# Optimization experiments

Hardware: AMD Instinct MI355X
Metric: run time of the kernel (lower is better)

The kernel has to match this reference:

```python
import jax, jax.numpy as jnp
import numpy as np

B, N, D = 4, 2048, 512      # batch, seq, dim_in
DK = DV = 512               # dim_k == dim_v (required by fc input width)
NH = 8
HK = DK // NH               # per-head dk == dv == 64
SCALE = 1.0 / np.sqrt(HK)
LN_EPS = 1e-5


def setup_inputs() -> dict:
    key = jax.random.key(0)
    ks = jax.random.split(key, 8)
    s = 0.02
    return {
        "x": jax.random.normal(ks[0], (B, N, D), dtype=jnp.float32),
        "Wq": jax.random.normal(ks[1], (D, DK), dtype=jnp.float32) * s,
        "Wk": jax.random.normal(ks[2], (D, DK), dtype=jnp.float32) * s,
        "Wv": jax.random.normal(ks[3], (D, DV), dtype=jnp.float32) * s,
        "Wf": jax.random.normal(ks[4], (2 * DK, D), dtype=jnp.float32) * s,
        "bf": jnp.zeros((D,), dtype=jnp.float32),
        "gamma": jnp.ones((D,), dtype=jnp.float32),
        "beta": jnp.zeros((D,), dtype=jnp.float32),
    }


def reference(x, Wq, Wk, Wv, Wf, bf, gamma, beta):
    b, n, _ = x.shape
    # projections -> [b, nh, n, hk]; q_c/q_f etc. are identical in the source,
    # so compute once.
    def proj(W):
        return jnp.einsum('bnd,dk->bnk', x, W).reshape(b, n, NH, -1).transpose(0, 2, 1, 3)
    q, k, v = proj(Wq), proj(Wk), proj(Wv)

    # conventional branch: softmax over n x n scores
    dist_c = jax.nn.softmax(jnp.einsum('bhqd,bhkd->bhqk', q, k) * SCALE, axis=-1)
    att_c = jnp.einsum('bhqk,bhkd->bhqd', dist_c, v)          # [b,nh,n,hk]
    att_c = att_c.transpose(0, 2, 1, 3).reshape(b, n, DV)

    # feature branch: softmax over dk x dk scores (linear-complexity variant)
    dist_f = jax.nn.softmax(jnp.einsum('bhnk,bhnq->bhkq', k, q) * SCALE, axis=-1)
    att_f = jnp.einsum('bhnd,bhdq->bhnq', v, dist_f)           # [b,nh,n,hk]
    att_f = att_f.transpose(0, 2, 1, 3).reshape(b, n, DV)

    att = jnp.concatenate([att_c, att_f], axis=2)              # [b,n,2*dk]
    out = jax.nn.relu(att @ Wf + bf)                           # dropout=eval (identity)
    out = out + x
    mu = jnp.mean(out, axis=-1, keepdims=True)
    var = jnp.var(out, axis=-1, keepdims=True)
    out = (out - mu) * jax.lax.rsqrt(var + LN_EPS) * gamma + beta
    return out
```

## Files before the change

### kernel.cpp

```cpp
#include <hip/hip_runtime.h>
#include <math.h>
#include <stdint.h>

#define B_   4
#define N_   2048
#define D_   512
#define DK_  512
#define NH_  8
#define HK_  64
#define LN_EPS_ 1e-5f
#define QS_  0.18033688011112042f

typedef unsigned short u16;
typedef __attribute__((ext_vector_type(8))) short short8;
typedef __attribute__((ext_vector_type(4))) float f32x4;
typedef __attribute__((ext_vector_type(8))) unsigned short u16x8;

__device__ __forceinline__ u16 f2bf(float x) {
    uint32_t u = __builtin_bit_cast(uint32_t, x);
    return (u16)((u + 0x7fffu + ((u >> 16) & 1u)) >> 16);
}
__device__ __forceinline__ u16 f2bf_fast(float x) {
    return (u16)((__builtin_bit_cast(uint32_t, x) + 0x8000u) >> 16);
}
__device__ __forceinline__ float b2f(u16 v) {
    return __builtin_bit_cast(float, (uint32_t)v << 16);
}
__device__ __forceinline__ uint32_t cvtpk_bf16(float lo, float hi) {
    uint32_t r;
    asm("v_cvt_pk_bf16_f32 %0, %1, %2" : "=v"(r) : "v"(lo), "v"(hi));
    return r;
}
__device__ __forceinline__ float exp2f_fast(float x) {
    return __builtin_amdgcn_exp2f(x);
}

__device__ __forceinline__ void gload16(const void* g, void* l) {
    __builtin_amdgcn_global_load_lds(
        reinterpret_cast<const __attribute__((address_space(1))) void*>(
            reinterpret_cast<uintptr_t>(g)),
        reinterpret_cast<__attribute__((address_space(3))) void*>(
            static_cast<uint32_t>(reinterpret_cast<uintptr_t>(l))),
        16, 0, 0);
}

__global__ __launch_bounds__(256) void prep_kernel(
    const float* __restrict__ x, const float* __restrict__ Wq,
    const float* __restrict__ Wk, const float* __restrict__ Wv,
    const float* __restrict__ Wf, u16* __restrict__ xb,
    u16* __restrict__ wqkvT, u16* __restrict__ wfT)
{
    __shared__ float t[32][33];
    const int bid = blockIdx.x, tid = threadIdx.x;
    if (bid < 2048) {
        const int i = (bid * 256 + tid) * 8;
        const float4 a = *reinterpret_cast<const float4*>(&x[i]);
        const float4 b = *reinterpret_cast<const float4*>(&x[i + 4]);
        u16x8 o;
        o[0] = f2bf(a.x); o[1] = f2bf(a.y); o[2] = f2bf(a.z); o[3] = f2bf(a.w);
        o[4] = f2bf(b.x); o[5] = f2bf(b.y); o[6] = f2bf(b.z); o[7] = f2bf(b.w);
        *reinterpret_cast<u16x8*>(&xb[i]) = o;
        return;
    }
    const float* W;
    u16* dst;
    int K, Nc, nt, kt;
    if (bid < 2816) {
        const int z = (bid - 2048) >> 8, rem = (bid - 2048) & 255;
        W = z == 0 ? Wq : (z == 1 ? Wk : Wv);
        dst = wqkvT + (size_t)z * 512 * 512;
        K = 512; Nc = 512;
        nt = (rem & 15) * 32; kt = (rem >> 4) * 32;
    } else {
        const int rem = bid - 2816;
        W = Wf; dst = wfT; K = 1024; Nc = 512;
        nt = (rem & 15) * 32; kt = (rem >> 4) * 32;
    }
    {
        const int r = tid >> 3, c0 = (tid & 7) * 4;
        const float4 v = *reinterpret_cast<const float4*>(
            &W[(size_t)(kt + r) * Nc + nt + c0]);
        t[r][c0] = v.x; t[r][c0 + 1] = v.y; t[r][c0 + 2] = v.z; t[r][c0 + 3] = v.w;
    }
    __syncthreads();
    {
        const int nidx = tid >> 3, kc = (tid & 7) * 4;
        u16 o[4];
        #pragma unroll
        for (int j = 0; j < 4; ++j) o[j] = f2bf(t[kc + j][nidx]);
        *reinterpret_cast<ushort4*>(&dst[(size_t)(nt + nidx) * K + kt + kc]) =
            make_ushort4(o[0], o[1], o[2], o[3]);
    }
}

template<int BM, int BN, int MODE>
__global__ __launch_bounds__(256) void gemm_bf16(
    const u16* __restrict__ A, const u16* __restrict__ Bt,
    u16* __restrict__ qb, u16* __restrict__ kb,
    u16* __restrict__ vb, u16* __restrict__ vt, int M, int Nc, int K,
    const float* __restrict__ bias, const float* __restrict__ resid)
{
    constexpr int MI = BM / 32, NI = BN / 32;
    constexpr int AL = BM / 32, BL = BN / 32;
    __shared__ u16 As[BM * 64];
    __shared__ u16 Bs[BN * 64];
    const int tid = threadIdx.x;
    const int lane = tid & 63, wave = tid >> 6;
    const int wm = wave >> 1, wn = wave & 1;
    const int l15 = lane & 15, lg = lane >> 4;

    const int nwg = gridDim.x;
    const int bid = ((int)blockIdx.x & 7) * (nwg >> 3) + ((int)blockIdx.x >> 3);
    const int ntiles = Nc / BN;
    const int nt = (bid % ntiles) * BN;
    const int mt = (bid / ntiles) * BM;

    f32x4 acc[MI][NI] = {};

    for (int kt = 0; kt < K; kt += 64) {
        __syncthreads();
        #pragma unroll
        for (int i = 0; i < AL; ++i) {
            const int ob = (wave * AL + i) * 1024;
            const int o = ob + lane * 16;
            const int row = o >> 7;
            const int inner = (o & 127) ^ ((row & 7) << 4);
            gload16((const char*)A + ((size_t)(mt + row) * K + kt) * 2 + inner,
                    (char*)As + ob);
        }
        #pragma unroll
        for (int i = 0; i < BL; ++i) {
            const int ob = (wave * BL + i) * 1024;
            const int o = ob + lane * 16;
            const int row = o >> 7;
            const int inner = (o & 127) ^ ((row & 7) << 4);
            gload16((const char*)Bt + ((size_t)(nt + row) * K + kt) * 2 + inner,
                    (char*)Bs + ob);
        }
        __syncthreads();
        #pragma unroll
        for (int ks = 0; ks < 2; ++ks) {
            const int kb2 = ks * 32 + lg * 8;
            short8 af[MI], bfr[NI];
            #pragma unroll
            for (int mi = 0; mi < MI; ++mi) {
                const int r = wm * (BM / 2) + mi * 16 + l15;
                af[mi] = *reinterpret_cast<const short8*>(
                    &As[r * 64 + (kb2 ^ ((r & 7) << 3))]);
            }
            #pragma unroll
            for (int ni = 0; ni < NI; ++ni) {
                const int r = wn * (BN / 2) + ni * 16 + l15;
                bfr[ni] = *reinterpret_cast<const short8*>(
                    &Bs[r * 64 + (kb2 ^ ((r & 7) << 3))]);
            }
            #pragma unroll
            for (int mi = 0; mi < MI; ++mi)
                #pragma unroll
                for (int ni = 0; ni < NI; ++ni)
                    acc[mi][ni] = __builtin_amdgcn_mfma_f32_16x16x32_bf16(
                        af[mi], bfr[ni], acc[mi][ni], 0, 0, 0);
        }
    }

    #pragma unroll
    for (int mi = 0; mi < MI; ++mi) {
        #pragma unroll
        for (int ni = 0; ni < NI; ++ni) {
            const int col = nt + wn * (BN / 2) + ni * 16 + l15;
            const int row0 = mt + wm * (BM / 2) + mi * 16 + lg * 4;
            if (MODE == 1) {
                if (col < 512) {
                    #pragma unroll
                    for (int jj = 0; jj < 4; ++jj)
                        qb[(size_t)(row0 + jj) * 512 + col] =
                            f2bf(acc[mi][ni][jj] * QS_);
                } else if (col < 1024) {
                    #pragma unroll
                    for (int jj = 0; jj < 4; ++jj)
                        kb[(size_t)(row0 + jj) * 512 + col - 512] =
                            f2bf(acc[mi][ni][jj]);
                } else {
                    const int dfull = col - 1024;
                    const int hh = dfull >> 6, dd = dfull & 63;
                    const int bb = row0 >> 11, nn = row0 & 2047;
                    u16 o4[4];
                    #pragma unroll
                    for (int jj = 0; jj < 4; ++jj) {
                        o4[jj] = f2bf(acc[mi][ni][jj]);
                        vb[(size_t)(row0 + jj) * 512 + dfull] = o4[jj];
                    }
                    *reinterpret_cast<ushort4*>(
                        &vt[(((size_t)(bb * NH_ + hh)) * HK_ + dd) * N_ + nn]) =
                        make_ushort4(o4[0], o4[1], o4[2], o4[3]);
                }
            } else {
                #pragma unroll
                for (int jj = 0; jj < 4; ++jj) {
                    const size_t row = (size_t)(row0 + jj);
                    float v = acc[mi][ni][jj];
                    v += bias[col];
                    v = fmaxf(v, 0.0f);
                    v += resid[row * Nc + col];
                    qb[row * Nc + col] = f2bf(v);
                }
            }
        }
    }
}

__global__ __launch_bounds__(256) void flash_featS_kernel(
    const u16* __restrict__ Qb, const u16* __restrict__ Kb,
    const u16* __restrict__ Vt, u16* __restrict__ att,
    float* __restrict__ partials)
{
    __shared__ u16 sh[24576];
    const int tid = threadIdx.x;
    const int lane = tid & 63, wave = tid >> 6;
    const int l15 = lane & 15, lg = lane >> 4;

    if ((int)blockIdx.x >= 512) {
        u16* KsT = sh;
        u16* QsT = sh + 4096;
        const int fid = (int)blockIdx.x - 512;
        const int ns = fid & 7, h = (fid >> 3) & 7, b = fid >> 6;
        const size_t hbase = (size_t)b * N_ * DK_ + (size_t)h * HK_;

        f32x4 acc[4] = {};
        for (int c = 0; c < 4; ++c) {
            const int n0 = ns * 256 + c * 64;
            __syncthreads();
            #pragma unroll
            for (int it = 0; it < 2; ++it) {
                const int idx = tid + it * 256;
                const int n = idx >> 3, d0 = (idx & 7) * 8;
                const u16x8 kv = *reinterpret_cast<const u16x8*>(
                    &Kb[hbase + (size_t)(n0 + n) * DK_ + d0]);
                const u16x8 qv = *reinterpret_cast<const u16x8*>(
                    &Qb[hbase + (size_t)(n0 + n) * DK_ + d0]);
                #pragma unroll
                for (int j = 0; j < 8; ++j) {
                    const int r = d0 + j;
                    const int cidx = n ^ ((r & 7) << 3);
                    KsT[r * 64 + cidx] = kv[j];
                    QsT[r * 64 + cidx] = qv[j];
                }
            }
            __syncthreads();
            #pragma unroll
            for (int ks = 0; ks < 2; ++ks) {
                const int kb2 = ks * 32 + lg * 8;
                const int ar = wave * 16 + l15;
                const short8 aK = *reinterpret_cast<const short8*>(
                    &KsT[ar * 64 + (kb2 ^ ((ar & 7) << 3))]);
                #pragma unroll
                for (int ni = 0; ni < 4; ++ni) {
                    const int br = ni * 16 + l15;
                    const short8 bQ = *reinterpret_cast<const short8*>(
                        &QsT[br * 64 + (kb2 ^ ((br & 7) << 3))]);
                    acc[ni] = __builtin_amdgcn_mfma_f32_16x16x32_bf16(
                        aK, bQ, acc[ni], 0, 0, 0);
                }
            }
        }
        const int bh = b * NH_ + h;
        #pragma unroll
        for (int ni = 0; ni < 4; ++ni)
            #pragma unroll
            for (int jj = 0; jj < 4; ++jj) {
                const int row = wave * 16 + lg * 4 + jj;
                partials[(((size_t)ns * 32 + bh) * 64 + row) * 64 + ni * 16 + l15] =
                    acc[ni][jj];
            }
        return;
    }

    u16* Ks0 = sh;
    u16* Ks1 = sh + 4096;
    u16* Vs0 = sh + 8192;
    u16* Vs1 = sh + 12288;
    u16* Ps  = sh + 16384;
    const int lbid = (((int)blockIdx.x & 7) << 6) + ((int)blockIdx.x >> 3);
    const int qt = lbid & 15, h = (lbid >> 4) & 7, b = lbid >> 7;

    short8 aq[2][2];
    #pragma unroll
    for (int qs = 0; qs < 2; ++qs) {
        const int qrow = qt * 128 + qs * 64 + wave * 16 + l15;
        const u16* qp = Qb + ((size_t)(b * N_ + qrow)) * DK_ + h * HK_ + lg * 8;
        aq[qs][0] = *reinterpret_cast<const short8*>(qp);
        aq[qs][1] = *reinterpret_cast<const short8*>(qp + 32);
    }
    short8 ones;
    #pragma unroll
    for (int i = 0; i < 8; ++i) ones[i] = (short)0x3F80;

    const u16* Kbase = Kb + (size_t)b * N_ * DK_ + (size_t)h * HK_;
    const u16* Vbase = Vt + ((size_t)(b * NH_ + h)) * HK_ * N_;
    unsigned long long* Ps64 = reinterpret_cast<unsigned long long*>(Ps);

    f32x4 o[2][5] = {};
    float m_[2] = {-1e30f, -1e30f};

#define STAGE(ktile, KBUF, VBUF) do {                                          \
    _Pragma("unroll")                                                          \
    for (int i_ = 0; i_ < 2; ++i_) {                                           \
        const int ob_ = (wave * 2 + i_) * 1024;                                \
        const int oo_ = ob_ + lane * 16;                                       \
        const int row_ = oo_ >> 7;                                             \
        const int inner_ = (oo_ & 127) ^ ((row_ & 7) << 4);                    \
        gload16((const char*)Kbase +                                           \
                    ((size_t)((ktile) * 64 + row_) * DK_) * 2 + inner_,        \
                (char*)(KBUF) + ob_);                                          \
        gload16((const char*)Vbase +                                           \
                    ((size_t)row_ * N_ + (ktile) * 64) * 2 + inner_,           \
                (char*)(VBUF) + ob_);                                          \
    }                                                                          \
} while (0)

#define FLASH_STEP(KBUF, VBUF) do {                                            \
    f32x4 s[2][4] = {};                                                        \
    __builtin_amdgcn_s_setprio(1);                                             \
    _Pragma("unroll")                                                          \
    for (int ks = 0; ks < 2; ++ks) {                                           \
        const int kb2 = ks * 32 + lg * 8;                                      \
        _Pragma("unroll")                                                      \
        for (int t = 0; t < 4; ++t) {                                          \
            const int r = t * 16 + l15;                                        \
            const short8 bk = *reinterpret_cast<const short8*>(                \
                &(KBUF)[r * 64 + (kb2 ^ ((r & 7) << 3))]);                     \
            s[0][t] = __builtin_amdgcn_mfma_f32_16x16x32_bf16(                 \
                bk, aq[0][ks], s[0][t], 0, 0, 0);                              \
            s[1][t] = __builtin_amdgcn_mfma_f32_16x16x32_bf16(                 \
                bk, aq[1][ks], s[1][t], 0, 0, 0);                              \
        }                                                                      \
    }                                                                          \
    __builtin_amdgcn_s_setprio(0);                                             \
    float rmax[2], cm;                                                         \
    _Pragma("unroll")                                                          \
    for (int qs = 0; qs < 2; ++qs) {                                           \
        float a0 = fmaxf(fmaxf(s[qs][0][0], s[qs][0][1]),                      \
                         fmaxf(s[qs][0][2], s[qs][0][3]));                     \
        float a1 = fmaxf(fmaxf(s[qs][1][0], s[qs][1][1]),                      \
                         fmaxf(s[qs][1][2], s[qs][1][3]));                     \
        float a2 = fmaxf(fmaxf(s[qs][2][0], s[qs][2][1]),                      \
                         fmaxf(s[qs][2][2], s[qs][2][3]));                     \
        float a3 = fmaxf(fmaxf(s[qs][3][0], s[qs][3][1]),                      \
                         fmaxf(s[qs][3][2], s[qs][3][3]));                     \
        rmax[qs] = fmaxf(fmaxf(a0, a1), fmaxf(a2, a3));                        \
    }                                                                          \
    cm = fmaxf(rmax[0] - m_[0], rmax[1] - m_[1]);                              \
    if (__any(cm > 8.0f)) {                                                    \
        _Pragma("unroll")                                                      \
        for (int qs = 0; qs < 2; ++qs) {                                       \
            float rm = rmax[qs];                                               \
            rm = fmaxf(rm, __shfl_xor(rm, 16));                                \
            rm = fmaxf(rm, __shfl_xor(rm, 32));                                \
            const float newm = fmaxf(m_[qs], rm);                              \
            const float fac = exp2f_fast(m_[qs] - newm);                       \
            m_[qs] = newm;                                                     \
            float facq[4];                                                     \
            _Pragma("unroll")                                                  \
            for (int jj = 0; jj < 4; ++jj)                                     \
                facq[jj] = __shfl(fac, lg * 4 + jj);                           \
            _Pragma("unroll")                                                  \
            for (int t = 0; t < 5; ++t)                                        \
                _Pragma("unroll")                                              \
                for (int jj = 0; jj < 4; ++jj)                                 \
                    o[qs][t][jj] *= facq[jj];                                  \
        }                                                                      \
    }                                                                          \
    _Pragma("unroll")                                                          \
    for (int qs = 0; qs < 2; ++qs) {                                           \
        const int prow = qs * 64 + wave * 16 + l15;                            \
        const int pb64 = prow * 16;                                            \
        const int sw1 = (prow & 7) << 1;                                       \
        _Pragma("unroll")                                                      \
        for (int t = 0; t < 4; ++t) {                                          \
            const float p0 = exp2f_fast(s[qs][t][0] - m_[qs]);                 \
            const float p1 = exp2f_fast(s[qs][t][1] - m_[qs]);                 \
            const float p2 = exp2f_fast(s[qs][t][2] - m_[qs]);                 \
            const float p3 = exp2f_fast(s[qs][t][3] - m_[qs]);                 \
            const uint32_t lo = cvtpk_bf16(p0, p1);                            \
            const uint32_t hi = cvtpk_bf16(p2, p3);                            \
            Ps64[pb64 + ((t * 4 + lg) ^ sw1)] =                                \
                (unsigned long long)lo | ((unsigned long long)hi << 32);       \
        }                                                                      \
    }                                                                          \
    __builtin_amdgcn_s_setprio(1);                                             \
    _Pragma("unroll")                                                          \
    for (int ks = 0; ks < 2; ++ks) {                                           \
        const int kb2 = ks * 32 + lg * 8;                                      \
        const int pr0 = wave * 16 + l15;                                       \
        const int pr1 = 64 + pr0;                                              \
        const short8 ap0 = *reinterpret_cast<const short8*>(                   \
            &Ps[pr0 * 64 + (kb2 ^ ((pr0 & 7) << 3))]);                         \
        const short8 ap1 = *reinterpret_cast<const short8*>(                   \
            &Ps[pr1 * 64 + (kb2 ^ ((pr1 & 7) << 3))]);                         \
        _Pragma("unroll")                                                      \
        for (int t = 0; t < 4; ++t) {                                          \
            const int dr = t * 16 + l15;                                       \
            const short8 bv = *reinterpret_cast<const short8*>(                \
                &(VBUF)[dr * 64 + (kb2 ^ ((dr & 7) << 3))]);                   \
            o[0][t] = __builtin_amdgcn_mfma_f32_16x16x32_bf16(                 \
                ap0, bv, o[0][t], 0, 0, 0);                                    \
            o[1][t] = __builtin_amdgcn_mfma_f32_16x16x32_bf16(                 \
                ap1, bv, o[1][t], 0, 0, 0);                                    \
        }                                                                      \
        o[0][4] = __builtin_amdgcn_mfma_f32_16x16x32_bf16(                     \
            ap0, ones, o[0][4], 0, 0, 0);                                      \
        o[1][4] = __builtin_amdgcn_mfma_f32_16x16x32_bf16(                     \
            ap1, ones, o[1][4], 0, 0, 0);                                      \
    }                                                                          \
    __builtin_amdgcn_s_setprio(0);                                             \
} while (0)

    STAGE(0, Ks0, Vs0);
    __syncthreads();

    #pragma unroll 1
    for (int kt = 0; kt < N_ / 64; kt += 2) {
        STAGE(kt + 1, Ks1, Vs1);
        FLASH_STEP(Ks0, Vs0);
        __syncthreads();
        if (kt + 2 < N_ / 64) STAGE(kt + 2, Ks0, Vs0);
        FLASH_STEP(Ks1, Vs1);
        __syncthreads();
    }
#undef STAGE
#undef FLASH_STEP

    #pragma unroll
    for (int qs = 0; qs < 2; ++qs)
        #pragma unroll
        for (int jj = 0; jj < 4; ++jj) {
            const float inv = 1.0f / o[qs][4][jj];
            const size_t row = (size_t)b * N_ + qt * 128 + qs * 64 + wave * 16 + lg * 4 + jj;
            #pragma unroll
            for (int t = 0; t < 4; ++t)
                att[row * (2 * DK_) + h * HK_ + t * 16 + l15] =
                    f2bf_fast(o[qs][t][jj] * inv);
        }
}

__global__ __launch_bounds__(256) void featSM_kernel(
    const float* __restrict__ partials, u16* __restrict__ distfT)
{
    const int bh = blockIdx.x, tid = threadIdx.x;
    const int r = tid >> 2, qq = tid & 3;
    float v[16];
    #pragma unroll
    for (int j = 0; j < 16; ++j) v[j] = 0.0f;
    for (int s = 0; s < 8; ++s) {
        const float4* pp = reinterpret_cast<const float4*>(
            &partials[(((size_t)s * 32 + bh) * 64 + r) * 64 + qq * 16]);
        #pragma unroll
        for (int j4 = 0; j4 < 4; ++j4) {
            const float4 a = pp[j4];
            v[j4 * 4 + 0] += a.x; v[j4 * 4 + 1] += a.y;
            v[j4 * 4 + 2] += a.z; v[j4 * 4 + 3] += a.w;
        }
    }
    float m = v[0];
    #pragma unroll
    for (int j = 1; j < 16; ++j) m = fmaxf(m, v[j]);
    m = fmaxf(m, __shfl_xor(m, 1));
    m = fmaxf(m, __shfl_xor(m, 2));
    float sum = 0.0f;
    #pragma unroll
    for (int j = 0; j < 16; ++j) { v[j] = exp2f_fast(v[j] - m); sum += v[j]; }
    sum += __shfl_xor(sum, 1);
    sum += __shfl_xor(sum, 2);
    const float inv = 1.0f / sum;
    #pragma unroll
    for (int j = 0; j < 16; ++j)
        distfT[(size_t)bh * 4096 + (qq * 16 + j) * 64 + r] = f2bf_fast(v[j] * inv);
}

__global__ __launch_bounds__(256) void featAV_mfma(
    const u16* __restrict__ V, const u16* __restrict__ distfT,
    u16* __restrict__ att)
{
    __shared__ u16 Bs[64 * 64];
    __shared__ u16 As[64 * 64];
    const int tid = threadIdx.x;
    const int lane = tid & 63, wave = tid >> 6;
    const int l15 = lane & 15, lg = lane >> 4;
    const int ns = blockIdx.x, h = blockIdx.y, b = blockIdx.z;
    const int bh = b * NH_ + h;

    #pragma unroll
    for (int it = 0; it < 2; ++it) {
        const int idx = tid + it * 256;
        const int r = idx >> 3, c0 = (idx & 7) * 8;
        const u16x8 dv = *reinterpret_cast<const u16x8*>(
            &distfT[(size_t)bh * 4096 + r * 64 + c0]);
        *reinterpret_cast<u16x8*>(&Bs[r * 64 + (c0 ^ ((r & 7) << 3))]) = dv;
    }

    for (int c = 0; c < 4; ++c) {
        const int n0 = ns * 256 + c * 64;
        __syncthreads();
        #pragma unroll
        for (int i = 0; i < 2; ++i) {
            const int ob = (wave * 2 + i) * 1024;
            const int o_ = ob + lane * 16;
            const int row = o_ >> 7;
            const int inner = (o_ & 127) ^ ((row & 7) << 4);
            gload16((const char*)V + ((size_t)(b * N_ + n0 + row) * DK_ + h * HK_) * 2 + inner,
                    (char*)As + ob);
        }
        __syncthreads();
        f32x4 acc[4] = {};
        #pragma unroll
        for (int ks = 0; ks < 2; ++ks) {
            const int kb2 = ks * 32 + lg * 8;
            const int ar = wave * 16 + l15;
            const short8 av = *reinterpret_cast<const short8*>(
                &As[ar * 64 + (kb2 ^ ((ar & 7) << 3))]);
            #pragma unroll
            for (int ni = 0; ni < 4; ++ni) {
                const int br = ni * 16 + l15;
                const short8 bd = *reinterpret_cast<const short8*>(
                    &Bs[br * 64 + (kb2 ^ ((br & 7) << 3))]);
                acc[ni] = __builtin_amdgcn_mfma_f32_16x16x32_bf16(av, bd, acc[ni], 0, 0, 0);
            }
        }
        #pragma unroll
        for (int ni = 0; ni < 4; ++ni)
            #pragma unroll
            for (int jj = 0; jj < 4; ++jj)
                att[((size_t)b * N_ + n0 + wave * 16 + lg * 4 + jj) * (2 * DK_)
                    + 512 + h * HK_ + ni * 16 + l15] = f2bf_fast(acc[ni][jj]);
    }
}

__global__ __launch_bounds__(256) void ln_kernel(
    const u16* __restrict__ fc, const float* __restrict__ gamma,
    const float* __restrict__ beta, float* __restrict__ out)
{
    const int row = blockIdx.x * 4 + (threadIdx.x >> 6);
    const int lane = threadIdx.x & 63;
    const int c = lane * 8;
    const u16x8 v = *reinterpret_cast<const u16x8*>(&fc[(size_t)row * D_ + c]);
    float f[8];
    float s = 0.0f, sq = 0.0f;
    #pragma unroll
    for (int j = 0; j < 8; ++j) {
        f[j] = b2f(v[j]);
        s += f[j];
        sq = fmaf(f[j], f[j], sq);
    }
    #pragma unroll
    for (int off = 32; off >= 1; off >>= 1) {
        s  += __shfl_xor(s, off);
        sq += __shfl_xor(sq, off);
    }
    const float mu = s * (1.0f / D_);
    const float var = sq * (1.0f / D_) - mu * mu;
    const float rstd = rsqrtf(var + LN_EPS_);
    const float4 g0 = *reinterpret_cast<const float4*>(&gamma[c]);
    const float4 g1 = *reinterpret_cast<const float4*>(&gamma[c + 4]);
    const float4 b0 = *reinterpret_cast<const float4*>(&beta[c]);
    const float4 b1 = *reinterpret_cast<const float4*>(&beta[c + 4]);
    const float gg[8] = {g0.x, g0.y, g0.z, g0.w, g1.x, g1.y, g1.z, g1.w};
    const float bb[8] = {b0.x, b0.y, b0.z, b0.w, b1.x, b1.y, b1.z, b1.w};
    float4 o0, o1;
    o0.x = (f[0] - mu) * rstd * gg[0] + bb[0];
    o0.y = (f[1] - mu) * rstd * gg[1] + bb[1];
    o0.z = (f[2] - mu) * rstd * gg[2] + bb[2];
    o0.w = (f[3] - mu) * rstd * gg[3] + bb[3];
    o1.x = (f[4] - mu) * rstd * gg[4] + bb[4];
    o1.y = (f[5] - mu) * rstd * gg[5] + bb[5];
    o1.z = (f[6] - mu) * rstd * gg[6] + bb[6];
    o1.w = (f[7] - mu) * rstd * gg[7] + bb[7];
    *reinterpret_cast<float4*>(&out[(size_t)row * D_ + c]) = o0;
    *reinterpret_cast<float4*>(&out[(size_t)row * D_ + c + 4]) = o1;
}

extern "C" void kernel_launch(void* const* d_in, const int* in_sizes, int n_in,
                              void* d_out, int out_size, void* d_ws, size_t ws_size,
                              hipStream_t stream)
{
    (void)in_sizes; (void)n_in; (void)out_size; (void)ws_size;
    const float* x     = (const float*)d_in[0];
    const float* Wq    = (const float*)d_in[1];
    const float* Wk    = (const float*)d_in[2];
    const float* Wv    = (const float*)d_in[3];
    const float* Wf    = (const float*)d_in[4];
    const float* bf    = (const float*)d_in[5];
    const float* gamma = (const float*)d_in[6];
    const float* beta  = (const float*)d_in[7];
    float* out = (float*)d_out;

    char* w = (char*)d_ws;
    const size_t SZE = (size_t)B_ * N_ * DK_;
    u16* xb     = (u16*)w;   w += SZE * 2;
    u16* wqkvT  = (u16*)w;   w += (size_t)1536 * 512 * 2;
    u16* wfT    = (u16*)w;   w += (size_t)512 * 1024 * 2;
    u16* qb     = (u16*)w;   w += SZE * 2;
    u16* kb     = (u16*)w;   w += SZE * 2;
    u16* vb     = (u16*)w;   w += SZE * 2;
    u16* vt     = (u16*)w;   w += SZE * 2;
    u16* attb   = (u16*)w;   w += SZE * 2 * 2;
    float* partials = (float*)w; w += (size_t)8 * 32 * 4096 * 4;
    u16* distfT = (u16*)w;   w += (size_t)32 * 4096 * 2;
    u16* fcout  = (u16*)w;

    const dim3 blk(256);
    const int M = B_ * N_;

    prep_kernel<<<dim3(3328), blk, 0, stream>>>(x, Wq, Wk, Wv, Wf, xb, wqkvT, wfT);

    gemm_bf16<128, 128, 1><<<dim3(768), blk, 0, stream>>>(
        xb, wqkvT, qb, kb, vb, vt, M, 1536, 512, nullptr, nullptr);

    flash_featS_kernel<<<dim3(768), blk, 0, stream>>>(qb, kb, vt, attb, partials);

    featSM_kernel<<<dim3(32), blk, 0, stream>>>(partials, distfT);
    featAV_mfma<<<dim3(8, NH_, B_), blk, 0, stream>>>(vb, distfT, attb);

    gemm_bf16<64, 128, 2><<<dim3(512), blk, 0, stream>>>(
        attb, wfT, fcout, nullptr, nullptr, nullptr, M, D_, 2 * DK_, bf, x);

    ln_kernel<<<dim3(2048), blk, 0, stream>>>(fcout, gamma, beta, out);
}
```

Baseline: 126.7 us.

## Software-pipeline flash attention: overlap next tile QK with current softmax and PV

```diff
diff --git a/kernel.cpp b/kernel.cpp
--- a/kernel.cpp
+++ b/kernel.cpp
@@ -275,10 +275,10 @@
         return;
     }
 
-    u16* Ks0 = sh;
-    u16* Ks1 = sh + 4096;
-    u16* Vs0 = sh + 8192;
-    u16* Vs1 = sh + 12288;
+    u16* kb0 = sh;
+    u16* kb1 = sh + 4096;
+    u16* vb0 = sh + 8192;
+    u16* vb1 = sh + 12288;
     u16* Ps  = sh + 16384;
     const int lbid = (((int)blockIdx.x & 7) << 6) + ((int)blockIdx.x >> 3);
     const int qt = lbid & 15, h = (lbid >> 4) & 7, b = lbid >> 7;
@@ -301,25 +301,36 @@
 
     f32x4 o[2][5] = {};
     float m_[2] = {-1e30f, -1e30f};
-
-#define STAGE(ktile, KBUF, VBUF) do {                                          \
+    f32x4 SA[2][4], SB[2][4];
+
+    const int ob0 = wave * 1024, oo0 = ob0 + lane * 16;
+    const int row0s = oo0 >> 7;
+    const int in0 = (oo0 & 127) ^ ((row0s & 7) << 4);
+
+#define STAGE_K(ktile, KBUF) do {                                              \
+    gload16((const char*)Kbase +                                               \
+                ((size_t)((ktile) * 64 + row0s) * DK_) * 2 + in0,              \
+            (char*)(KBUF) + ob0);                                              \
+    gload16((const char*)Kbase +                                               \
+                ((size_t)((ktile) * 64 + 32 + row0s) * DK_) * 2 + in0,         \
+            (char*)(KBUF) + 4096 + ob0);                                       \
+} while (0)
+
+#define STAGE_V(ktile, VBUF) do {                                              \
+    gload16((const char*)Vbase +                                               \
+                ((size_t)row0s * N_ + (ktile) * 64) * 2 + in0,                 \
+            (char*)(VBUF) + ob0);                                              \
+    gload16((const char*)Vbase +                                               \
+                ((size_t)(32 + row0s) * N_ + (ktile) * 64) * 2 + in0,          \
+            (char*)(VBUF) + 4096 + ob0);                                       \
+} while (0)
+
+#define QK_STEP(S, KBUF) do {                                                  \
     _Pragma("unroll")                                                          \
-    for (int i_ = 0; i_ < 2; ++i_) {                                           \
-        const int ob_ = (wave * 2 + i_) * 1024;                                \
-        const int oo_ = ob_ + lane * 16;                                       \
-        const int row_ = oo_ >> 7;                                             \
-        const int inner_ = (oo_ & 127) ^ ((row_ & 7) << 4);                    \
-        gload16((const char*)Kbase +                                           \
-                    ((size_t)((ktile) * 64 + row_) * DK_) * 2 + inner_,        \
-                (char*)(KBUF) + ob_);                                          \
-        gload16((const char*)Vbase +                                           \
-                    ((size_t)row_ * N_ + (ktile) * 64) * 2 + inner_,           \
-                (char*)(VBUF) + ob_);                                          \
-    }                                                                          \
-} while (0)
-
-#define FLASH_STEP(KBUF, VBUF) do {                                            \
-    f32x4 s[2][4] = {};                                                        \
+    for (int qs = 0; qs < 2; ++qs)                                             \
+        _Pragma("unroll")                                                      \
+        for (int t = 0; t < 4; ++t)                                            \
+            S[qs][t] = (f32x4){0.0f, 0.0f, 0.0f, 0.0f};                        \
     __builtin_amdgcn_s_setprio(1);                                             \
     _Pragma("unroll")                                                          \
     for (int ks = 0; ks < 2; ++ks) {                                           \
@@ -329,24 +340,27 @@
             const int r = t * 16 + l15;                                        \
             const short8 bk = *reinterpret_cast<const short8*>(                \
                 &(KBUF)[r * 64 + (kb2 ^ ((r & 7) << 3))]);                     \
-            s[0][t] = __builtin_amdgcn_mfma_f32_16x16x32_bf16(                 \
-                bk, aq[0][ks], s[0][t], 0, 0, 0);                              \
-            s[1][t] = __builtin_amdgcn_mfma_f32_16x16x32_bf16(                 \
-                bk, aq[1][ks], s[1][t], 0, 0, 0);                              \
+            S[0][t] = __builtin_amdgcn_mfma_f32_16x16x32_bf16(                 \
+                bk, aq[0][ks], S[0][t], 0, 0, 0);                              \
+            S[1][t] = __builtin_amdgcn_mfma_f32_16x16x32_bf16(                 \
+                bk, aq[1][ks], S[1][t], 0, 0, 0);                              \
         }                                                                      \
     }                                                                          \
     __builtin_amdgcn_s_setprio(0);                                             \
+} while (0)
+
+#define SMPV_STEP(S, VBUF) do {                                                \
     float rmax[2], cm;                                                         \
     _Pragma("unroll")                                                          \
     for (int qs = 0; qs < 2; ++qs) {                                           \
-        float a0 = fmaxf(fmaxf(s[qs][0][0], s[qs][0][1]),                      \
-                         fmaxf(s[qs][0][2], s[qs][0][3]));                     \
-        float a1 = fmaxf(fmaxf(s[qs][1][0], s[qs][1][1]),                      \
-                         fmaxf(s[qs][1][2], s[qs][1][3]));                     \
-        float a2 = fmaxf(fmaxf(s[qs][2][0], s[qs][2][1]),                      \
-                         fmaxf(s[qs][2][2], s[qs][2][3]));                     \
-        float a3 = fmaxf(fmaxf(s[qs][3][0], s[qs][3][1]),                      \
-                         fmaxf(s[qs][3][2], s[qs][3][3]));                     \
+        float a0 = fmaxf(fmaxf(S[qs][0][0], S[qs][0][1]),                      \
+                         fmaxf(S[qs][0][2], S[qs][0][3]));                     \
+        float a1 = fmaxf(fmaxf(S[qs][1][0], S[qs][1][1]),                      \
+                         fmaxf(S[qs][1][2], S[qs][1][3]));                     \
+        float a2 = fmaxf(fmaxf(S[qs][2][0], S[qs][2][1]),                      \
+                         fmaxf(S[qs][2][2], S[qs][2][3]));                     \
+        float a3 = fmaxf(fmaxf(S[qs][3][0], S[qs][3][1]),                      \
+                         fmaxf(S[qs][3][2], S[qs][3][3]));                     \
         rmax[qs] = fmaxf(fmaxf(a0, a1), fmaxf(a2, a3));                        \
     }                                                                          \
     cm = fmaxf(rmax[0] - m_[0], rmax[1] - m_[1]);                              \
@@ -377,10 +391,10 @@
         const int sw1 = (prow & 7) << 1;                                       \
         _Pragma("unroll")                                                      \
         for (int t = 0; t < 4; ++t) {                                          \
-            const float p0 = exp2f_fast(s[qs][t][0] - m_[qs]);                 \
-            const float p1 = exp2f_fast(s[qs][t][1] - m_[qs]);                 \
-            const float p2 = exp2f_fast(s[qs][t][2] - m_[qs]);                 \
-            const float p3 = exp2f_fast(s[qs][t][3] - m_[qs]);                 \
+            const float p0 = exp2f_fast(S[qs][t][0] - m_[qs]);                 \
+            const float p1 = exp2f_fast(S[qs][t][1] - m_[qs]);                 \
+            const float p2 = exp2f_fast(S[qs][t][2] - m_[qs]);                 \
+            const float p3 = exp2f_fast(S[qs][t][3] - m_[qs]);                 \
             const uint32_t lo = cvtpk_bf16(p0, p1);                            \
             const uint32_t hi = cvtpk_bf16(p2, p3);                            \
             Ps64[pb64 + ((t * 4 + lg) ^ sw1)] =                                \
@@ -415,20 +429,36 @@
     __builtin_amdgcn_s_setprio(0);                                             \
 } while (0)
 
-    STAGE(0, Ks0, Vs0);
+    STAGE_K(0, kb0);
+    STAGE_K(1, kb1);
+    STAGE_V(0, vb0);
     __syncthreads();
+    QK_STEP(SA, kb0);
 
     #pragma unroll 1
-    for (int kt = 0; kt < N_ / 64; kt += 2) {
-        STAGE(kt + 1, Ks1, Vs1);
-        FLASH_STEP(Ks0, Vs0);
+    for (int t2 = 0; t2 < 30; t2 += 2) {
         __syncthreads();
-        if (kt + 2 < N_ / 64) STAGE(kt + 2, Ks0, Vs0);
-        FLASH_STEP(Ks1, Vs1);
+        STAGE_K(t2 + 2, kb0);
+        STAGE_V(t2 + 1, vb1);
+        QK_STEP(SB, kb1);
+        SMPV_STEP(SA, vb0);
         __syncthreads();
-    }
-#undef STAGE
-#undef FLASH_STEP
+        STAGE_K(t2 + 3, kb1);
+        STAGE_V(t2 + 2, vb0);
+        QK_STEP(SA, kb0);
+        SMPV_STEP(SB, vb1);
+    }
+    __syncthreads();
+    STAGE_V(31, vb1);
+    QK_STEP(SB, kb1);
+    SMPV_STEP(SA, vb0);
+    __syncthreads();
+    SMPV_STEP(SB, vb1);
+
+#undef STAGE_K
+#undef STAGE_V
+#undef QK_STEP
+#undef SMPV_STEP
 
     #pragma unroll
     for (int qs = 0; qs < 2; ++qs)
```

Result: no change. 126.2 us (median of 2 runs) (-0.4%).
